# Performance work log

Hardware: AMD Instinct MI355X
Metric: run time of the kernel (lower is better)

## Reference

```python
import jax, jax.numpy as jnp
import numpy as np

N_NODES = 100000
N_EDGES = 1600000


def gcn_conv(x, W, b, src, dst, norm):
    # x: [N, Fin] -> [N, Fout]; transform-then-aggregate (GCNConv order)
    h = x @ W
    msg = h[src] * norm[:, None]            # gather + degree-normalized messages
    agg = jax.ops.segment_sum(msg, dst, num_segments=N_NODES)  # scatter-add
    return agg + b


def setup_inputs() -> dict:
    key = jax.random.key(0)
    ks = jax.random.split(key, 6)
    x = jax.random.normal(ks[0], (N_NODES, 50), dtype=jnp.float32)
    edge_index = jax.random.randint(ks[1], (2, N_EDGES), 0, N_NODES, dtype=jnp.int32)
    def glorot(k, fin, fout):
        s = jnp.sqrt(2.0 / (fin + fout)).astype(jnp.float32)
        return jax.random.normal(k, (fin, fout), dtype=jnp.float32) * s
    return {
        "x": x,
        "edge_index": edge_index,
        "W1": glorot(ks[2], 50, 128),  "b1": jnp.zeros((128,), jnp.float32),
        "W2": glorot(ks[3], 128, 128), "b2": jnp.zeros((128,), jnp.float32),
        "W3": glorot(ks[4], 128, 128), "b3": jnp.zeros((128,), jnp.float32),
        "W4": glorot(ks[5], 128, 121), "b4": jnp.zeros((121,), jnp.float32),
    }


def reference(x, edge_index, W1, b1, W2, b2, W3, b3, W4, b4):
    # GCNConv with self-loops and symmetric normalization D^-1/2 (A+I) D^-1/2
    loop = jnp.arange(N_NODES, dtype=edge_index.dtype)
    src = jnp.concatenate([edge_index[0], loop])
    dst = jnp.concatenate([edge_index[1], loop])
    deg = jax.ops.segment_sum(jnp.ones_like(dst, dtype=x.dtype), dst,
                              num_segments=N_NODES)
    dis = jnp.where(deg > 0, jax.lax.rsqrt(jnp.maximum(deg, 1e-12)), 0.0)
    norm = dis[src] * dis[dst]               # [E + N]

    h = jax.nn.relu(gcn_conv(x, W1, b1, src, dst, norm))
    h = jax.nn.relu(gcn_conv(h, W2, b2, src, dst, norm))
    h = jax.nn.relu(gcn_conv(h, W3, b3, src, dst, norm))
    out = gcn_conv(h, W4, b4, src, dst, norm)
    return jax.nn.sigmoid(out)
```

## Files before the change

### kernel.cpp

```cpp
#include <hip/hip_runtime.h>
#include <math.h>

#define NNODES 100000
#define BSHIFT 9
#define NBKT ((NNODES + (1 << BSHIFT) - 1) >> BSHIFT)
#define CAPB 10240
#define CHUNK 2048

typedef _Float16 f16x8 __attribute__((ext_vector_type(8)));
typedef _Float16 f16x2 __attribute__((ext_vector_type(2)));
typedef float f32x4 __attribute__((ext_vector_type(4)));

__global__ __launch_bounds__(256) void bin_kernel(
        const int* __restrict__ eidx, int E,
        unsigned* __restrict__ bedge, int* __restrict__ bcur) {
    __shared__ int hist[256];
    __shared__ int scanx[256];
    __shared__ int gbase[256];
    __shared__ unsigned stage[CHUNK];
    int tid = threadIdx.x;
    int base = blockIdx.x * CHUNK;
    if (base >= E) return;
    int m = min(CHUNK, E - base);
    hist[tid] = 0;
    __syncthreads();
    unsigned pk[8];
    int b[8], r[8];
#pragma unroll
    for (int j = 0; j < 8; ++j) {
        int rel = j * 256 + tid;
        bool ok = rel < m;
        int e = base + (ok ? rel : 0);
        int s = eidx[e];
        int d = eidx[E + e];
        b[j] = d >> BSHIFT;
        pk[j] = ((unsigned)(d & ((1 << BSHIFT) - 1)) << 17) | (unsigned)s;
        r[j] = ok ? atomicAdd(&hist[b[j]], 1) : -1;
    }
    __syncthreads();
    int h = hist[tid];
    scanx[tid] = h;
    __syncthreads();
    for (int st = 1; st < 256; st <<= 1) {
        int y = (tid >= st) ? scanx[tid - st] : 0;
        __syncthreads();
        scanx[tid] += y;
        __syncthreads();
    }
    int excl = scanx[tid] - h;
    if (h > 0) gbase[tid] = atomicAdd(&bcur[tid], h);
    __syncthreads();
    scanx[tid] = excl;
    __syncthreads();
#pragma unroll
    for (int j = 0; j < 8; ++j)
        if (r[j] >= 0) stage[scanx[b[j]] + r[j]] = pk[j];
    __syncthreads();
    for (int i = tid; i < m; i += 256) {
        int lo = 0, hi = NBKT - 1;
        while (lo < hi) {
            int mid = (lo + hi + 1) >> 1;
            if (scanx[mid] <= i) lo = mid; else hi = mid - 1;
        }
        int idx = gbase[lo] + (i - scanx[lo]);
        if (idx < CAPB) bedge[(size_t)lo * CAPB + idx] = stage[i];
    }
}

__global__ __launch_bounds__(512) void count2_kernel(
        const unsigned* __restrict__ bedge, const int* __restrict__ bcur,
        int* __restrict__ counts, int n) {
    __shared__ int h[512];
    int b = blockIdx.x;
    int tid = threadIdx.x;
    h[tid] = 0;
    __syncthreads();
    int cnt = min(bcur[b], CAPB);
    const unsigned* e = bedge + (size_t)b * CAPB;
    for (int i = tid; i < cnt; i += 512) atomicAdd(&h[e[i] >> 17], 1);
    __syncthreads();
    int node = b * 512 + tid;
    if (node < n) counts[node] = h[tid];
}

__global__ void dis_kernel(const int* __restrict__ counts, float* __restrict__ dis, int n) {
    int i = blockIdx.x * 256 + threadIdx.x;
    if (i < n) dis[i] = rsqrtf((float)(counts[i] + 1));
    else if (i == n) dis[i] = 0.f;
}

__global__ void scan_local(const int* __restrict__ counts, int* __restrict__ offs,
                           int* __restrict__ bsums, int n) {
    __shared__ int tsum[256];
    int t = threadIdx.x;
    int base = blockIdx.x * 1024 + t * 4;
    int v0 = (base + 0 < n) ? ((counts[base + 0] + 7) & ~7) : 0;
    int v1 = (base + 1 < n) ? ((counts[base + 1] + 7) & ~7) : 0;
    int v2 = (base + 2 < n) ? ((counts[base + 2] + 7) & ~7) : 0;
    int v3 = (base + 3 < n) ? ((counts[base + 3] + 7) & ~7) : 0;
    tsum[t] = v0 + v1 + v2 + v3;
    __syncthreads();
    for (int d = 1; d < 256; d <<= 1) {
        int x = tsum[t];
        int y = (t >= d) ? tsum[t - d] : 0;
        __syncthreads();
        tsum[t] = x + y;
        __syncthreads();
    }
    int prev = (t > 0) ? tsum[t - 1] : 0;
    if (base + 0 < n) offs[base + 0] = prev;
    if (base + 1 < n) offs[base + 1] = prev + v0;
    if (base + 2 < n) offs[base + 2] = prev + v0 + v1;
    if (base + 3 < n) offs[base + 3] = prev + v0 + v1 + v2;
    if (t == 255) bsums[blockIdx.x] = tsum[255];
}

__global__ void scan_bsums(int* __restrict__ bsums, int nb) {
    __shared__ int s[128];
    int t = threadIdx.x;
    s[t] = (t < nb) ? bsums[t] : 0;
    __syncthreads();
    for (int d = 1; d < 128; d <<= 1) {
        int x = s[t];
        int y = (t >= d) ? s[t - d] : 0;
        __syncthreads();
        s[t] = x + y;
        __syncthreads();
    }
    int excl = (t > 0) ? s[t - 1] : 0;
    if (t < nb) bsums[t] = excl;
}

__global__ void add_base(int* __restrict__ offs, const int* __restrict__ bsums, int n) {
    int i = blockIdx.x * 256 + threadIdx.x;
    if (i < n) offs[i] += bsums[i >> 10];
}

__global__ __launch_bounds__(512) void fill2_kernel(
        const unsigned* __restrict__ bedge, const int* __restrict__ bcur,
        const int* __restrict__ offs, int* __restrict__ csrc, int n) {
    __shared__ int lofs[512];
    __shared__ int lcur[512];
    int b = blockIdx.x;
    int tid = threadIdx.x;
    int node = b * 512 + tid;
    lofs[tid] = (node < n) ? offs[node] : 0;
    lcur[tid] = 0;
    __syncthreads();
    int cnt = min(bcur[b], CAPB);
    const unsigned* e = bedge + (size_t)b * CAPB;
    for (int i = tid; i < cnt; i += 512) {
        unsigned pk = e[i];
        int dl = pk >> 17;
        int p = lofs[dl] + atomicAdd(&lcur[dl], 1);
        csrc[p] = (int)(pk & 0x1FFFFu);
    }
}

__global__ void pad_kernel(const int* __restrict__ offs, const int* __restrict__ counts,
                           int* __restrict__ csrc, int n) {
    int i = blockIdx.x * 256 + threadIdx.x;
    if (i >= n) return;
    int c = counts[i];
    int p = (c + 7) & ~7;
    int o = offs[i];
    for (int j = c; j < p; ++j) csrc[o + j] = NNODES;
}

__global__ void cast_kernel(const float* __restrict__ src, _Float16* __restrict__ dst, int n2) {
    int i = blockIdx.x * 256 + threadIdx.x;
    if (i < n2) {
        float2 v = *(const float2*)&src[i * 2];
        f16x2 h;
        h.x = (_Float16)v.x;
        h.y = (_Float16)v.y;
        *(f16x2*)&dst[i * 2] = h;
    }
}


__global__ __launch_bounds__(256) void agg128_kernel(
        const f16x2* __restrict__ in, f16x2* __restrict__ out,
        const int* __restrict__ offs, const int* __restrict__ counts,
        const int* __restrict__ csrc, const float* __restrict__ dis, int n) {
    int wid = blockIdx.x * (blockDim.x >> 6) + (threadIdx.x >> 6);
    int lane = threadIdx.x & 63;
    if (wid >= n) return;
    float dd = dis[wid];
    f16x2 self = in[(size_t)wid * 64 + lane];
    float a0 = dd * dd * (float)self.x;
    float a1 = dd * dd * (float)self.y;
    int off = offs[wid];
    int pcnt = (counts[wid] + 7) & ~7;
    for (int j = 0; j < pcnt; j += 8) {
        int4 s0 = *(const int4*)&csrc[off + j];
        int4 s1 = *(const int4*)&csrc[off + j + 4];
        float v0 = dis[s0.x] * dd, v1 = dis[s0.y] * dd;
        float v2 = dis[s0.z] * dd, v3 = dis[s0.w] * dd;
        float v4 = dis[s1.x] * dd, v5 = dis[s1.y] * dd;
        float v6 = dis[s1.z] * dd, v7 = dis[s1.w] * dd;
        f16x2 r0 = in[(size_t)s0.x * 64 + lane];
        f16x2 r1 = in[(size_t)s0.y * 64 + lane];
        f16x2 r2 = in[(size_t)s0.z * 64 + lane];
        f16x2 r3 = in[(size_t)s0.w * 64 + lane];
        f16x2 r4 = in[(size_t)s1.x * 64 + lane];
        f16x2 r5 = in[(size_t)s1.y * 64 + lane];
        f16x2 r6 = in[(size_t)s1.z * 64 + lane];
        f16x2 r7 = in[(size_t)s1.w * 64 + lane];
        a0 = fmaf(v0, (float)r0.x, a0); a1 = fmaf(v0, (float)r0.y, a1);
        a0 = fmaf(v1, (float)r1.x, a0); a1 = fmaf(v1, (float)r1.y, a1);
        a0 = fmaf(v2, (float)r2.x, a0); a1 = fmaf(v2, (float)r2.y, a1);
        a0 = fmaf(v3, (float)r3.x, a0); a1 = fmaf(v3, (float)r3.y, a1);
        a0 = fmaf(v4, (float)r4.x, a0); a1 = fmaf(v4, (float)r4.y, a1);
        a0 = fmaf(v5, (float)r5.x, a0); a1 = fmaf(v5, (float)r5.y, a1);
        a0 = fmaf(v6, (float)r6.x, a0); a1 = fmaf(v6, (float)r6.y, a1);
        a0 = fmaf(v7, (float)r7.x, a0); a1 = fmaf(v7, (float)r7.y, a1);
    }
    f16x2 o;
    o.x = (_Float16)a0;
    o.y = (_Float16)a1;
    out[(size_t)wid * 64 + lane] = o;
}

__global__ __launch_bounds__(256) void agg50_kernel(
        const _Float16* __restrict__ in, _Float16* __restrict__ out,
        const int* __restrict__ offs, const int* __restrict__ counts,
        const int* __restrict__ csrc, const float* __restrict__ dis, int n) {
    int wid = blockIdx.x * (blockDim.x >> 6) + (threadIdx.x >> 6);
    int lane = threadIdx.x & 63;
    if (wid >= n) return;
    float dd = dis[wid];
    float acc = 0.f;
    if (lane < 50) acc = dd * dd * (float)in[(size_t)wid * 50 + lane];
    int off = offs[wid];
    int pcnt = (counts[wid] + 7) & ~7;
    for (int j = 0; j < pcnt; j += 8) {
        int4 s0 = *(const int4*)&csrc[off + j];
        int4 s1 = *(const int4*)&csrc[off + j + 4];
        float v0 = dis[s0.x] * dd, v1 = dis[s0.y] * dd;
        float v2 = dis[s0.z] * dd, v3 = dis[s0.w] * dd;
        float v4 = dis[s1.x] * dd, v5 = dis[s1.y] * dd;
        float v6 = dis[s1.z] * dd, v7 = dis[s1.w] * dd;
        if (lane < 50) {
            float r0 = (float)in[(size_t)s0.x * 50 + lane];
            float r1 = (float)in[(size_t)s0.y * 50 + lane];
            float r2 = (float)in[(size_t)s0.z * 50 + lane];
            float r3 = (float)in[(size_t)s0.w * 50 + lane];
            float r4 = (float)in[(size_t)s1.x * 50 + lane];
            float r5 = (float)in[(size_t)s1.y * 50 + lane];
            float r6 = (float)in[(size_t)s1.z * 50 + lane];
            float r7 = (float)in[(size_t)s1.w * 50 + lane];
            acc = fmaf(v0, r0, acc);
            acc = fmaf(v1, r1, acc);
            acc = fmaf(v2, r2, acc);
            acc = fmaf(v3, r3, acc);
            acc = fmaf(v4, r4, acc);
            acc = fmaf(v5, r5, acc);
            acc = fmaf(v6, r6, acc);
            acc = fmaf(v7, r7, acc);
        }
    }
    out[(size_t)wid * 64 + lane] = (lane < 50) ? (_Float16)acc : (_Float16)0.f;
}

__global__ void wfrag_kernel(const float* __restrict__ W, f16x8* __restrict__ frag,
                             int FIN, int FOUT, int KCN, int CTN) {
    int idx = blockIdx.x * 256 + threadIdx.x;
    int tot = KCN * CTN * 64;
    if (idx >= tot) return;
    int lane = idx & 63;
    int ct = (idx >> 6) % CTN;
    int kc = (idx >> 6) / CTN;
    int c = ct * 16 + (lane & 15);
    int kb = kc * 32 + (lane >> 4) * 8;
    f16x8 v;
#pragma unroll
    for (int j = 0; j < 8; ++j) {
        int k = kb + j;
        float w = (k < FIN && c < FOUT) ? W[(size_t)k * FOUT + c] : 0.f;
        v[j] = (_Float16)w;
    }
    frag[idx] = v;
}

template <int KCN, int CTN, int ACT, typename OT>
__global__ __launch_bounds__(256) void gemm_mfma(
        const _Float16* __restrict__ A, int lda,
        const f16x8* __restrict__ wfrag,
        const float* __restrict__ bias, int fout,
        OT* __restrict__ out, int ldo, int n) {
    int wid = blockIdx.x * 4 + (threadIdx.x >> 6);
    int lane = threadIdx.x & 63;
    int rbase = wid * 16;
    if (rbase >= n) return;
    int r = lane & 15;
    int g = lane >> 4;
    int gr = rbase + r;
    const _Float16* arow = A + (size_t)((gr < n) ? gr : 0) * lda + g * 8;

    f32x4 acc[CTN];
#pragma unroll
    for (int ct = 0; ct < CTN; ++ct) acc[ct] = (f32x4){0.f, 0.f, 0.f, 0.f};

#pragma unroll
    for (int kc = 0; kc < KCN; ++kc) {
        f16x8 a = *(const f16x8*)(arow + kc * 32);
        const f16x8* wk = wfrag + (size_t)(kc * CTN) * 64 + lane;
#pragma unroll
        for (int ct = 0; ct < CTN; ++ct) {
            f16x8 b = wk[(size_t)ct * 64];
            acc[ct] = __builtin_amdgcn_mfma_f32_16x16x32_f16(a, b, acc[ct], 0, 0, 0);
        }
    }

    int orow0 = rbase + g * 4;
#pragma unroll
    for (int ct = 0; ct < CTN; ++ct) {
        int col = ct * 16 + (lane & 15);
        if (col >= fout) continue;
        float bv = bias[col];
#pragma unroll
        for (int q = 0; q < 4; ++q) {
            int orow = orow0 + q;
            if (orow >= n) continue;
            float v = acc[ct][q] + bv;
            if (ACT == 0) v = fmaxf(v, 0.f);
            else v = 1.f / (1.f + __expf(-v));
            out[(size_t)orow * ldo + col] = (OT)v;
        }
    }
}

extern "C" void kernel_launch(void* const* d_in, const int* in_sizes, int n_in,
                              void* d_out, int out_size, void* d_ws, size_t ws_size,
                              hipStream_t stream) {
    const float* x = (const float*)d_in[0];
    const int* eidx = (const int*)d_in[1];
    const float* W1 = (const float*)d_in[2];
    const float* b1 = (const float*)d_in[3];
    const float* W2 = (const float*)d_in[4];
    const float* b2 = (const float*)d_in[5];
    const float* W3 = (const float*)d_in[6];
    const float* b3 = (const float*)d_in[7];
    const float* W4 = (const float*)d_in[8];
    const float* b4 = (const float*)d_in[9];
    float* out = (float*)d_out;

    const int N = NNODES;
    const int E = in_sizes[1] / 2;
    const size_t PE = (size_t)E + 8u * N;

    char* ws = (char*)d_ws;
    size_t off = 0;
    auto alloc = [&](size_t bytes) -> char* {
        char* p = ws + off;
        off = (off + bytes + 255) & ~(size_t)255;
        return p;
    };
    float* dis = (float*)alloc((size_t)(N + 1) * 4);
    int* counts = (int*)alloc((size_t)N * 4);
    int* offs = (int*)alloc((size_t)N * 4);
    int* bsums = (int*)alloc(128 * 4);
    int* bcur = (int*)alloc(256 * 4);
    int* csrc = (int*)alloc(PE * 4);
    _Float16* aggH = (_Float16*)alloc((size_t)N * 128 * 2);
    _Float16* hH = (_Float16*)alloc((size_t)(N + 1) * 128 * 2);
    _Float16* x16 = (_Float16*)alloc((size_t)(N + 1) * 50 * 2);
    f16x8* wf1 = (f16x8*)alloc((size_t)2 * 8 * 64 * 16);
    f16x8* wf2 = (f16x8*)alloc((size_t)4 * 8 * 64 * 16);
    f16x8* wf3 = (f16x8*)alloc((size_t)4 * 8 * 64 * 16);
    f16x8* wf4 = (f16x8*)alloc((size_t)4 * 8 * 64 * 16);
    unsigned* bedge = (unsigned*)aggH;

    hipMemsetAsync(bcur, 0, 256 * 4, stream);

    wfrag_kernel<<<(2 * 8 * 64 + 255) / 256, 256, 0, stream>>>(W1, wf1, 50, 128, 2, 8);
    wfrag_kernel<<<(4 * 8 * 64 + 255) / 256, 256, 0, stream>>>(W2, wf2, 128, 128, 4, 8);
    wfrag_kernel<<<(4 * 8 * 64 + 255) / 256, 256, 0, stream>>>(W3, wf3, 128, 128, 4, 8);
    wfrag_kernel<<<(4 * 8 * 64 + 255) / 256, 256, 0, stream>>>(W4, wf4, 128, 121, 4, 8);

    bin_kernel<<<(E + CHUNK - 1) / CHUNK, 256, 0, stream>>>(eidx, E, bedge, bcur);
    count2_kernel<<<NBKT, 512, 0, stream>>>(bedge, bcur, counts, N);
    dis_kernel<<<(N + 256) / 256, 256, 0, stream>>>(counts, dis, N);
    int nb = (N + 1023) / 1024;
    scan_local<<<nb, 256, 0, stream>>>(counts, offs, bsums, N);
    scan_bsums<<<1, 128, 0, stream>>>(bsums, nb);
    add_base<<<(N + 255) / 256, 256, 0, stream>>>(offs, bsums, N);
    fill2_kernel<<<NBKT, 512, 0, stream>>>(bedge, bcur, offs, csrc, N);
    pad_kernel<<<(N + 255) / 256, 256, 0, stream>>>(offs, counts, csrc, N);

    int nx2 = N * 50 / 2;
    cast_kernel<<<(nx2 + 255) / 256, 256, 0, stream>>>(x, x16, nx2);

    int gblocks = ((N + 15) / 16 + 3) / 4;
    agg50_kernel<<<(N + 3) / 4, 256, 0, stream>>>(x16, aggH, offs, counts, csrc, dis, N);
    gemm_mfma<2, 8, 0, _Float16><<<gblocks, 256, 0, stream>>>(aggH, 64, wf1, b1, 128, hH, 128, N);
    agg128_kernel<<<(N + 3) / 4, 256, 0, stream>>>((const f16x2*)hH, (f16x2*)aggH, offs, counts, csrc, dis, N);
    gemm_mfma<4, 8, 0, _Float16><<<gblocks, 256, 0, stream>>>(aggH, 128, wf2, b2, 128, hH, 128, N);
    agg128_kernel<<<(N + 3) / 4, 256, 0, stream>>>((const f16x2*)hH, (f16x2*)aggH, offs, counts, csrc, dis, N);
    gemm_mfma<4, 8, 0, _Float16><<<gblocks, 256, 0, stream>>>(aggH, 128, wf3, b3, 128, hH, 128, N);
    agg128_kernel<<<(N + 3) / 4, 256, 0, stream>>>((const f16x2*)hH, (f16x2*)aggH, offs, counts, csrc, dis, N);
    gemm_mfma<4, 8, 1, float><<<gblocks, 256, 0, stream>>>(aggH, 128, wf4, b4, 121, out, 121, N);
}
```

Before: 429.1 us.

## Fuse neighbor aggregation with MFMA GEMM per 16-node block via swizzled LDS

Each layer's aggregation and dense transform now run in one kernel: a block aggregates 16 nodes (4 per wave) into a swizzled shared-memory tile, then each wave computes 32 output columns with MFMA. This removes the round trip of the intermediate aggregated buffer through global memory and halves the kernel launches. Input x is padded to 64 halfs per row so the first layer reuses the same path. In exchange, each wave processes 4 nodes serially, which may reduce memory-level parallelism in the latency-bound gather, and the grid assumes N is divisible by 16.

```diff
diff --git a/kernel.cpp b/kernel.cpp
--- a/kernel.cpp
+++ b/kernel.cpp
@@ -167,100 +167,19 @@
     for (int j = c; j < p; ++j) csrc[o + j] = NNODES;
 }
 
-__global__ void cast_kernel(const float* __restrict__ src, _Float16* __restrict__ dst, int n2) {
-    int i = blockIdx.x * 256 + threadIdx.x;
-    if (i < n2) {
-        float2 v = *(const float2*)&src[i * 2];
-        f16x2 h;
-        h.x = (_Float16)v.x;
-        h.y = (_Float16)v.y;
-        *(f16x2*)&dst[i * 2] = h;
-    }
-}
-
-
-__global__ __launch_bounds__(256) void agg128_kernel(
-        const f16x2* __restrict__ in, f16x2* __restrict__ out,
-        const int* __restrict__ offs, const int* __restrict__ counts,
-        const int* __restrict__ csrc, const float* __restrict__ dis, int n) {
-    int wid = blockIdx.x * (blockDim.x >> 6) + (threadIdx.x >> 6);
-    int lane = threadIdx.x & 63;
-    if (wid >= n) return;
-    float dd = dis[wid];
-    f16x2 self = in[(size_t)wid * 64 + lane];
-    float a0 = dd * dd * (float)self.x;
-    float a1 = dd * dd * (float)self.y;
-    int off = offs[wid];
-    int pcnt = (counts[wid] + 7) & ~7;
-    for (int j = 0; j < pcnt; j += 8) {
-        int4 s0 = *(const int4*)&csrc[off + j];
-        int4 s1 = *(const int4*)&csrc[off + j + 4];
-        float v0 = dis[s0.x] * dd, v1 = dis[s0.y] * dd;
-        float v2 = dis[s0.z] * dd, v3 = dis[s0.w] * dd;
-        float v4 = dis[s1.x] * dd, v5 = dis[s1.y] * dd;
-        float v6 = dis[s1.z] * dd, v7 = dis[s1.w] * dd;
-        f16x2 r0 = in[(size_t)s0.x * 64 + lane];
-        f16x2 r1 = in[(size_t)s0.y * 64 + lane];
-        f16x2 r2 = in[(size_t)s0.z * 64 + lane];
-        f16x2 r3 = in[(size_t)s0.w * 64 + lane];
-        f16x2 r4 = in[(size_t)s1.x * 64 + lane];
-        f16x2 r5 = in[(size_t)s1.y * 64 + lane];
-        f16x2 r6 = in[(size_t)s1.z * 64 + lane];
-        f16x2 r7 = in[(size_t)s1.w * 64 + lane];
-        a0 = fmaf(v0, (float)r0.x, a0); a1 = fmaf(v0, (float)r0.y, a1);
-        a0 = fmaf(v1, (float)r1.x, a0); a1 = fmaf(v1, (float)r1.y, a1);
-        a0 = fmaf(v2, (float)r2.x, a0); a1 = fmaf(v2, (float)r2.y, a1);
-        a0 = fmaf(v3, (float)r3.x, a0); a1 = fmaf(v3, (float)r3.y, a1);
-        a0 = fmaf(v4, (float)r4.x, a0); a1 = fmaf(v4, (float)r4.y, a1);
-        a0 = fmaf(v5, (float)r5.x, a0); a1 = fmaf(v5, (float)r5.y, a1);
-        a0 = fmaf(v6, (float)r6.x, a0); a1 = fmaf(v6, (float)r6.y, a1);
-        a0 = fmaf(v7, (float)r7.x, a0); a1 = fmaf(v7, (float)r7.y, a1);
-    }
-    f16x2 o;
-    o.x = (_Float16)a0;
-    o.y = (_Float16)a1;
-    out[(size_t)wid * 64 + lane] = o;
-}
-
-__global__ __launch_bounds__(256) void agg50_kernel(
-        const _Float16* __restrict__ in, _Float16* __restrict__ out,
-        const int* __restrict__ offs, const int* __restrict__ counts,
-        const int* __restrict__ csrc, const float* __restrict__ dis, int n) {
-    int wid = blockIdx.x * (blockDim.x >> 6) + (threadIdx.x >> 6);
-    int lane = threadIdx.x & 63;
-    if (wid >= n) return;
-    float dd = dis[wid];
-    float acc = 0.f;
-    if (lane < 50) acc = dd * dd * (float)in[(size_t)wid * 50 + lane];
-    int off = offs[wid];
-    int pcnt = (counts[wid] + 7) & ~7;
-    for (int j = 0; j < pcnt; j += 8) {
-        int4 s0 = *(const int4*)&csrc[off + j];
-        int4 s1 = *(const int4*)&csrc[off + j + 4];
-        float v0 = dis[s0.x] * dd, v1 = dis[s0.y] * dd;
-        float v2 = dis[s0.z] * dd, v3 = dis[s0.w] * dd;
-        float v4 = dis[s1.x] * dd, v5 = dis[s1.y] * dd;
-        float v6 = dis[s1.z] * dd, v7 = dis[s1.w] * dd;
-        if (lane < 50) {
-            float r0 = (float)in[(size_t)s0.x * 50 + lane];
-            float r1 = (float)in[(size_t)s0.y * 50 + lane];
-            float r2 = (float)in[(size_t)s0.z * 50 + lane];
-            float r3 = (float)in[(size_t)s0.w * 50 + lane];
-            float r4 = (float)in[(size_t)s1.x * 50 + lane];
-            float r5 = (float)in[(size_t)s1.y * 50 + lane];
-            float r6 = (float)in[(size_t)s1.z * 50 + lane];
-            float r7 = (float)in[(size_t)s1.w * 50 + lane];
-            acc = fmaf(v0, r0, acc);
-            acc = fmaf(v1, r1, acc);
-            acc = fmaf(v2, r2, acc);
-            acc = fmaf(v3, r3, acc);
-            acc = fmaf(v4, r4, acc);
-            acc = fmaf(v5, r5, acc);
-            acc = fmaf(v6, r6, acc);
-            acc = fmaf(v7, r7, acc);
-        }
-    }
-    out[(size_t)wid * 64 + lane] = (lane < 50) ? (_Float16)acc : (_Float16)0.f;
+__global__ void cast_pad_kernel(const float* __restrict__ src, _Float16* __restrict__ dst,
+                                int n) {
+    int t = blockIdx.x * 256 + threadIdx.x;
+    if (t >= n * 32) return;
+    int node = t >> 5;
+    int cp = t & 31;
+    int c = cp * 2;
+    float v0 = (c < 50) ? src[(size_t)node * 50 + c] : 0.f;
+    float v1 = (c + 1 < 50) ? src[(size_t)node * 50 + c + 1] : 0.f;
+    f16x2 h;
+    h.x = (_Float16)v0;
+    h.y = (_Float16)v1;
+    *(f16x2*)&dst[(size_t)node * 64 + c] = h;
 }
 
 __global__ void wfrag_kernel(const float* __restrict__ W, f16x8* __restrict__ frag,
@@ -283,47 +202,91 @@
     frag[idx] = v;
 }
 
-template <int KCN, int CTN, int ACT, typename OT>
-__global__ __launch_bounds__(256) void gemm_mfma(
-        const _Float16* __restrict__ A, int lda,
-        const f16x8* __restrict__ wfrag,
+template <int KCN, int ACT, typename OT>
+__global__ __launch_bounds__(256) void fused_kernel(
+        const f16x2* __restrict__ in, const int* __restrict__ offs,
+        const int* __restrict__ counts, const int* __restrict__ csrc,
+        const float* __restrict__ dis, const f16x8* __restrict__ wfrag,
         const float* __restrict__ bias, int fout,
         OT* __restrict__ out, int ldo, int n) {
-    int wid = blockIdx.x * 4 + (threadIdx.x >> 6);
-    int lane = threadIdx.x & 63;
-    int rbase = wid * 16;
-    if (rbase >= n) return;
-    int r = lane & 15;
-    int g = lane >> 4;
-    int gr = rbase + r;
-    const _Float16* arow = A + (size_t)((gr < n) ? gr : 0) * lda + g * 8;
-
-    f32x4 acc[CTN];
-#pragma unroll
-    for (int ct = 0; ct < CTN; ++ct) acc[ct] = (f32x4){0.f, 0.f, 0.f, 0.f};
-
+    constexpr int K = KCN * 32;
+    constexpr int ROWB = K * 2;
+    constexpr int HW = K / 2;
+    __shared__ __align__(16) unsigned char sA[16 * ROWB];
+    int tid = threadIdx.x;
+    int wv = tid >> 6, lane = tid & 63;
+    int nb = blockIdx.x * 16;
+    bool act = lane < HW;
+
+#pragma unroll 1
+    for (int s = 0; s < 4; ++s) {
+        int node = nb + wv * 4 + s;
+        float dd = dis[node];
+        float a0 = 0.f, a1 = 0.f;
+        if (act) {
+            f16x2 self = in[(size_t)node * HW + lane];
+            a0 = dd * dd * (float)self.x;
+            a1 = dd * dd * (float)self.y;
+        }
+        int off = offs[node];
+        int pcnt = (counts[node] + 7) & ~7;
+        for (int j = 0; j < pcnt; j += 8) {
+            int4 s0 = *(const int4*)&csrc[off + j];
+            int4 s1 = *(const int4*)&csrc[off + j + 4];
+            float v0 = dis[s0.x] * dd, v1 = dis[s0.y] * dd;
+            float v2 = dis[s0.z] * dd, v3 = dis[s0.w] * dd;
+            float v4 = dis[s1.x] * dd, v5 = dis[s1.y] * dd;
+            float v6 = dis[s1.z] * dd, v7 = dis[s1.w] * dd;
+            if (act) {
+                f16x2 r0 = in[(size_t)s0.x * HW + lane];
+                f16x2 r1 = in[(size_t)s0.y * HW + lane];
+                f16x2 r2 = in[(size_t)s0.z * HW + lane];
+                f16x2 r3 = in[(size_t)s0.w * HW + lane];
+                f16x2 r4 = in[(size_t)s1.x * HW + lane];
+                f16x2 r5 = in[(size_t)s1.y * HW + lane];
+                f16x2 r6 = in[(size_t)s1.z * HW + lane];
+                f16x2 r7 = in[(size_t)s1.w * HW + lane];
+                a0 = fmaf(v0, (float)r0.x, a0); a1 = fmaf(v0, (float)r0.y, a1);
+                a0 = fmaf(v1, (float)r1.x, a0); a1 = fmaf(v1, (float)r1.y, a1);
+                a0 = fmaf(v2, (float)r2.x, a0); a1 = fmaf(v2, (float)r2.y, a1);
+                a0 = fmaf(v3, (float)r3.x, a0); a1 = fmaf(v3, (float)r3.y, a1);
+                a0 = fmaf(v4, (float)r4.x, a0); a1 = fmaf(v4, (float)r4.y, a1);
+                a0 = fmaf(v5, (float)r5.x, a0); a1 = fmaf(v5, (float)r5.y, a1);
+                a0 = fmaf(v6, (float)r6.x, a0); a1 = fmaf(v6, (float)r6.y, a1);
+                a0 = fmaf(v7, (float)r7.x, a0); a1 = fmaf(v7, (float)r7.y, a1);
+            }
+        }
+        int r = wv * 4 + s;
+        if (act) {
+            f16x2 o;
+            o.x = (_Float16)a0;
+            o.y = (_Float16)a1;
+            *(f16x2*)(sA + r * ROWB + ((lane * 4) ^ ((r & 7) << 4))) = o;
+        }
+    }
+    __syncthreads();
+
+    int r = lane & 15, g = lane >> 4;
+    f32x4 acc[2];
+    acc[0] = (f32x4){0.f, 0.f, 0.f, 0.f};
+    acc[1] = (f32x4){0.f, 0.f, 0.f, 0.f};
 #pragma unroll
     for (int kc = 0; kc < KCN; ++kc) {
-        f16x8 a = *(const f16x8*)(arow + kc * 32);
-        const f16x8* wk = wfrag + (size_t)(kc * CTN) * 64 + lane;
-#pragma unroll
-        for (int ct = 0; ct < CTN; ++ct) {
-            f16x8 b = wk[(size_t)ct * 64];
-            acc[ct] = __builtin_amdgcn_mfma_f32_16x16x32_f16(a, b, acc[ct], 0, 0, 0);
-        }
-    }
-
-    int orow0 = rbase + g * 4;
-#pragma unroll
-    for (int ct = 0; ct < CTN; ++ct) {
-        int col = ct * 16 + (lane & 15);
+        f16x8 a = *(const f16x8*)(sA + r * ROWB + ((kc * 64 + g * 16) ^ ((r & 7) << 4)));
+        f16x8 b0 = wfrag[(size_t)(kc * 8 + wv * 2 + 0) * 64 + lane];
+        f16x8 b1 = wfrag[(size_t)(kc * 8 + wv * 2 + 1) * 64 + lane];
+        acc[0] = __builtin_amdgcn_mfma_f32_16x16x32_f16(a, b0, acc[0], 0, 0, 0);
+        acc[1] = __builtin_amdgcn_mfma_f32_16x16x32_f16(a, b1, acc[1], 0, 0, 0);
+    }
+#pragma unroll
+    for (int c = 0; c < 2; ++c) {
+        int col = (wv * 2 + c) * 16 + r;
         if (col >= fout) continue;
         float bv = bias[col];
 #pragma unroll
         for (int q = 0; q < 4; ++q) {
-            int orow = orow0 + q;
-            if (orow >= n) continue;
-            float v = acc[ct][q] + bv;
+            int orow = nb + g * 4 + q;
+            float v = acc[c][q] + bv;
             if (ACT == 0) v = fmaxf(v, 0.f);
             else v = 1.f / (1.f + __expf(-v));
             out[(size_t)orow * ldo + col] = (OT)v;
@@ -363,14 +326,14 @@
     int* bsums = (int*)alloc(128 * 4);
     int* bcur = (int*)alloc(256 * 4);
     int* csrc = (int*)alloc(PE * 4);
-    _Float16* aggH = (_Float16*)alloc((size_t)N * 128 * 2);
-    _Float16* hH = (_Float16*)alloc((size_t)(N + 1) * 128 * 2);
-    _Float16* x16 = (_Float16*)alloc((size_t)(N + 1) * 50 * 2);
+    _Float16* hA = (_Float16*)alloc((size_t)(N + 1) * 128 * 2);
+    _Float16* hB = (_Float16*)alloc((size_t)(N + 1) * 128 * 2);
+    _Float16* x16 = (_Float16*)alloc((size_t)(N + 1) * 64 * 2);
     f16x8* wf1 = (f16x8*)alloc((size_t)2 * 8 * 64 * 16);
     f16x8* wf2 = (f16x8*)alloc((size_t)4 * 8 * 64 * 16);
     f16x8* wf3 = (f16x8*)alloc((size_t)4 * 8 * 64 * 16);
     f16x8* wf4 = (f16x8*)alloc((size_t)4 * 8 * 64 * 16);
-    unsigned* bedge = (unsigned*)aggH;
+    unsigned* bedge = (unsigned*)hB;
 
     hipMemsetAsync(bcur, 0, 256 * 4, stream);
 
@@ -389,16 +352,15 @@
     fill2_kernel<<<NBKT, 512, 0, stream>>>(bedge, bcur, offs, csrc, N);
     pad_kernel<<<(N + 255) / 256, 256, 0, stream>>>(offs, counts, csrc, N);
 
-    int nx2 = N * 50 / 2;
-    cast_kernel<<<(nx2 + 255) / 256, 256, 0, stream>>>(x, x16, nx2);
-
-    int gblocks = ((N + 15) / 16 + 3) / 4;
-    agg50_kernel<<<(N + 3) / 4, 256, 0, stream>>>(x16, aggH, offs, counts, csrc, dis, N);
-    gemm_mfma<2, 8, 0, _Float16><<<gblocks, 256, 0, stream>>>(aggH, 64, wf1, b1, 128, hH, 128, N);
-    agg128_kernel<<<(N + 3) / 4, 256, 0, stream>>>((const f16x2*)hH, (f16x2*)aggH, offs, counts, csrc, dis, N);
-    gemm_mfma<4, 8, 0, _Float16><<<gblocks, 256, 0, stream>>>(aggH, 128, wf2, b2, 128, hH, 128, N);
-    agg128_kernel<<<(N + 3) / 4, 256, 0, stream>>>((const f16x2*)hH, (f16x2*)aggH, offs, counts, csrc, dis, N);
-    gemm_mfma<4, 8, 0, _Float16><<<gblocks, 256, 0, stream>>>(aggH, 128, wf3, b3, 128, hH, 128, N);
-    agg128_kernel<<<(N + 3) / 4, 256, 0, stream>>>((const f16x2*)hH, (f16x2*)aggH, offs, counts, csrc, dis, N);
-    gemm_mfma<4, 8, 1, float><<<gblocks, 256, 0, stream>>>(aggH, 128, wf4, b4, 121, out, 121, N);
-}
+    cast_pad_kernel<<<(N * 32 + 255) / 256, 256, 0, stream>>>(x, x16, N);
+
+    int fblocks = N / 16;
+    fused_kernel<2, 0, _Float16><<<fblocks, 256, 0, stream>>>(
+        (const f16x2*)x16, offs, counts, csrc, dis, wf1, b1, 128, hA, 128, N);
+    fused_kernel<4, 0, _Float16><<<fblocks, 256, 0, stream>>>(
+        (const f16x2*)hA, offs, counts, csrc, dis, wf2, b2, 128, hB, 128, N);
+    fused_kernel<4, 0, _Float16><<<fblocks, 256, 0, stream>>>(
+        (const f16x2*)hB, offs, counts, csrc, dis, wf3, b3, 128, hA, 128, N);
+    fused_kernel<4, 1, float><<<fblocks, 256, 0, stream>>>(
+        (const f16x2*)hA, offs, counts, csrc, dis, wf4, b4, 121, out, 121, N);
+}
```

Result: faster. 378.3 us (-11.8%).
